# Kernel tuning notes

Measured on AMD Instinct MI355X. Metric: run time of the kernel, lower is better.

The kernel has to match this reference:

```python
import jax, jax.numpy as jnp
import numpy as np

ALPHA = 0.2      # leaky_alpha
GRAPH_ITR = 2    # graph_itr
ENC_LEN = 250    # output_begin_idx = encoder_sequence.shape[1]


def _char_embedding(ids, emb, conv_w, conv_b):
    # ids: [B,N,Wl] int -> char-CNN: embed, conv1d over word dim, relu, max-pool
    x = emb[ids]                                      # [B,N,Wl,E]
    B, N, Wl, E = x.shape
    x = x.reshape(B * N, Wl, E).transpose(0, 2, 1)    # [B*N, E, Wl]
    y = jax.lax.conv_general_dilated(x, conv_w, (1,), [(2, 2)],
                                     dimension_numbers=('NCH', 'OIH', 'NCH'))
    y = jax.nn.relu(y + conv_b[None, :, None])        # [B*N, F, Wl]
    return y.max(axis=2).reshape(B, N, -1)            # [B,N,F]


def _dynamic_graph(x, W0a, W0b, b0, W1, b1, Wout, bout):
    # Pairwise MLP on concat(x_i, x_j); first layer computed as split matmuls
    # so the [B,N,N,2d] concat is never materialized.
    hi = jnp.einsum('bnd,de->bne', x, W0a)            # [B,N,d]
    hj = jnp.einsum('bnd,de->bne', x, W0b)            # [B,N,d]
    h = jax.nn.relu(hi[:, :, None, :] + hj[:, None, :, :] + b0)   # [B,N,N,d]
    h = jax.nn.relu(jnp.einsum('bnme,ef->bnmf', h, W1) + b1)      # [B,N,N,d]
    return jax.nn.sigmoid(jnp.einsum('bnme,e->bnm', h, Wout[:, 0]) + bout[0])


def _gat(x, adj, W, a1, a2):
    # Multi-head GAT: per-head projection, additive attention, adjacency-masked softmax.
    Wh = jnp.einsum('bnd,hdk->bhnk', x, W)            # [B,H,N,hid]
    f1 = jnp.einsum('bhnk,hk->bhn', Wh, a1)
    f2 = jnp.einsum('bhnk,hk->bhn', Wh, a2)
    e = jax.nn.leaky_relu(f1[:, :, :, None] + f2[:, :, None, :], ALPHA)  # [B,H,N,N]
    e = jnp.where(adj[:, None, :, :] > 0, e, -9e15)
    attn = jax.nn.softmax(e, axis=-1)
    h = jax.nn.elu(jnp.einsum('bhnm,bhmk->bhnk', attn, Wh))
    B, H, N, K = h.shape
    return h.transpose(0, 2, 1, 3).reshape(B, N, H * K)  # concat heads -> [B,N,d]


def setup_inputs() -> dict:
    key = jax.random.key(0)
    ks = jax.random.split(key, 20)
    B, Le, Ld, Wl = 2, 250, 150, 16
    Vin, E, F, K = 128, 64, 128, 5
    H, hid, Vout = 8, 32, 5000
    d = H * hid  # 256
    s = lambda k, sh: jax.random.normal(k, sh, dtype=jnp.float32) * 0.05
    return {
        'encoder_sequence': jax.random.randint(ks[0], (B, Le, Wl), 0, Vin),
        'initial_decoder_sequence': jax.random.randint(ks[1], (B, Ld, Wl), 0, Vin),
        'fixed_graph': jax.random.randint(ks[2], (B, Le + Ld, Le + Ld), 0, 2),
        'char_emb': s(ks[3], (Vin, E)),
        'conv_w': s(ks[4], (F, E, K)),
        'conv_b': jnp.zeros((F,), jnp.float32),
        'hst_W': s(ks[5], (F, d)),
        'hst_b': jnp.zeros((d,), jnp.float32),
        'dg_W0a': s(ks[6], (d, d)),
        'dg_W0b': s(ks[7], (d, d)),
        'dg_b0': jnp.zeros((d,), jnp.float32),
        'dg_W1': s(ks[8], (d, d)),
        'dg_b1': jnp.zeros((d,), jnp.float32),
        'dg_Wout': s(ks[9], (d, 1)),
        'dg_bout': jnp.zeros((1,), jnp.float32),
        'att_W': s(ks[10], (H, d, hid)),
        'att_a1': s(ks[11], (H, hid)),
        'att_a2': s(ks[12], (H, hid)),
        'out_W': s(ks[13], (d, Vout)),
        'out_b': jnp.zeros((Vout,), jnp.float32),
    }


def reference(encoder_sequence, initial_decoder_sequence, fixed_graph,
              char_emb, conv_w, conv_b, hst_W, hst_b,
              dg_W0a, dg_W0b, dg_b0, dg_W1, dg_b1, dg_Wout, dg_bout,
              att_W, att_a1, att_a2, out_W, out_b):
    ids = jnp.concatenate([encoder_sequence, initial_decoder_sequence], axis=1)  # [B,N,Wl]
    x = _char_embedding(ids, char_emb, conv_w, conv_b)    # [B,N,F]
    x = x @ hst_W + hst_b                                 # [B,N,d]
    fixed = fixed_graph.astype(jnp.float32)
    for _ in range(GRAPH_ITR):
        dyn = _dynamic_graph(x, dg_W0a, dg_W0b, dg_b0, dg_W1, dg_b1, dg_Wout, dg_bout)
        adj = jnp.clip(dyn + fixed, 0.0, 1.0)             # combine dynamic + fixed graph
        x = _gat(x, adj, att_W, att_a1, att_a2)
    return x[:, ENC_LEN:, :] @ out_W + out_b              # [B, dec_len, Vout]
```

## Files before the change

kernel.cpp:

```cpp
#include <hip/hip_runtime.h>
#include <hip/hip_bf16.h>
#include <math.h>


__device__ __forceinline__ float bf2f_raw(unsigned int u) {
    union { unsigned int i; float f; } cv; cv.i = u << 16; return cv.f;
}

__global__ void k_table(const float* emb, const float* convw, float* T) {
    int v = blockIdx.x, f = threadIdx.x;
    __shared__ float er[64];
    if (f < 64) er[f] = emb[v * 64 + f];
    __syncthreads();
    float acc[5] = {0.f, 0.f, 0.f, 0.f, 0.f};
    const float* w = convw + f * 320;
    for (int e = 0; e < 64; ++e) {
        float xe = er[e];
#pragma unroll
        for (int k = 0; k < 5; ++k) acc[k] += xe * w[e * 5 + k];
    }
#pragma unroll
    for (int k = 0; k < 5; ++k) T[(k * 128 + v) * 128 + f] = acc[k];
}

__global__ void k_conv(const int* enc, const int* dec, const float* convb,
                       const float* T, float* xc) {
    int w = blockIdx.x;
    int b = w / 400, n = w % 400;
    __shared__ int ids[16];
    int f = threadIdx.x;
    if (f < 16) {
        ids[f] = (n < 250) ? enc[(b * 250 + n) * 16 + f]
                           : dec[(b * 150 + (n - 250)) * 16 + f];
    }
    __syncthreads();
    float best = -1e30f;
    for (int p = 0; p < 16; ++p) {
        float s = 0.f;
#pragma unroll
        for (int k = 0; k < 5; ++k) {
            int q = p + k - 2;
            if (q >= 0 && q < 16) s += T[(k * 128 + ids[q]) * 128 + f];
        }
        best = fmaxf(best, s);
    }
    xc[w * 128 + f] = fmaxf(best + convb[f], 0.f);
}

__global__ void k_hst(const float* xc, const float* W, const float* bias, float* x) {
    int w = blockIdx.x, t = threadIdx.x;
    __shared__ float xr[128];
    if (t < 128) xr[t] = xc[w * 128 + t];
    __syncthreads();
    float acc = bias[t];
    for (int c = 0; c < 128; ++c) acc += xr[c] * W[c * 256 + t];
    x[w * 256 + t] = acc;
}

__global__ __launch_bounds__(256) void k_wh(const float* x, const float* attW,
                                            const float* a1g, const float* a2g,
                                            float* Wh, float* f1, float* f2) {
    int blk = blockIdx.x, t = threadIdx.x;
    int w0 = blk * 2;
    int h = t >> 5, k = t & 31;
    __shared__ float xr[2][256];
    for (int i = t; i < 512; i += 256) xr[i >> 8][i & 255] = x[w0 * 256 + i];
    __syncthreads();
    float acc0 = 0.f, acc1 = 0.f;
    const float* Wp = attW + h * 8192 + k;
#pragma unroll 8
    for (int d = 0; d < 256; ++d) {
        float wv = Wp[d * 32];
        acc0 += xr[0][d] * wv;
        acc1 += xr[1][d] * wv;
    }
    float a1v = a1g[t], a2v = a2g[t];
    int b = w0 / 400;
    int bh = b * 8 + h;
    float accs[2] = {acc0, acc1};
#pragma unroll
    for (int rw = 0; rw < 2; ++rw) {
        int n = (w0 + rw) % 400;
        Wh[(bh * 400 + n) * 32 + k] = accs[rw];
        float v1 = accs[rw] * a1v, v2 = accs[rw] * a2v;
#pragma unroll
        for (int mm = 16; mm >= 1; mm >>= 1) {
            v1 += __shfl_xor(v1, mm, 64);
            v2 += __shfl_xor(v2, mm, 64);
        }
        if (k == 0) { f1[bh * 400 + n] = v1; f2[bh * 400 + n] = v2; }
    }
}

#define WST 36
__global__ __launch_bounds__(256) void k_attn(const float* Wh, const float* f1g,
                                              const float* f2g, float* xout) {
    int tile = blockIdx.x, bh = blockIdx.y;
    int b = bh >> 3, h = bh & 7;
    int t = threadIdx.x;
    int n0 = tile * 16;
    __shared__ float Whl[400 * WST];
    __shared__ float f2l[400];
    __shared__ float pl[4][400];
    __shared__ float f1l[16];
    __shared__ float red[4][8][4][4];
    __shared__ float sred[2][4][4];
    __shared__ float wmax[4];

    const float4* Whg4 = (const float4*)(Wh + bh * 12800);
    for (int i = t; i < 3200; i += 256) {
        float4 v = Whg4[i];
        int m = i >> 3, k4 = i & 7;
        *(float4*)&Whl[m * WST + k4 * 4] = v;
    }
    float fm = -1e30f;
    for (int m = t; m < 400; m += 256) {
        float v = f2g[bh * 400 + m];
        f2l[m] = v;
        fm = fmaxf(fm, v);
    }
    if (t < 16) f1l[t] = f1g[bh * 400 + n0 + t];
#pragma unroll
    for (int mm = 32; mm >= 1; mm >>= 1) fm = fmaxf(fm, __shfl_xor(fm, mm, 64));
    if ((t & 63) == 0) wmax[t >> 6] = fm;
    __syncthreads();
    float fmax2 = fmaxf(fmaxf(wmax[0], wmax[1]), fmaxf(wmax[2], wmax[3]));

    int g = t & 7, kq = (t >> 3) & 7, wv = t >> 6;
    int gm = g + 8 * wv;
    for (int it = 0; it < 4; ++it) {
        float ps[4];
#pragma unroll
        for (int rr = 0; rr < 4; ++rr) {
            float f1n = f1l[it * 4 + rr];
            float rowm = f1n + fmax2;
            rowm = rowm > 0.f ? rowm : 0.2f * rowm;
            float p_s = 0.f;
            for (int m = t; m < 400; m += 256) {
                float e = f1n + f2l[m];
                e = e > 0.f ? e : 0.2f * e;
                float p = __expf(e - rowm);
                pl[rr][m] = p;
                p_s += p;
            }
            ps[rr] = p_s;
        }
#pragma unroll
        for (int rr = 0; rr < 4; ++rr) {
            float v = ps[rr];
#pragma unroll
            for (int mm = 32; mm >= 1; mm >>= 1) v += __shfl_xor(v, mm, 64);
            if ((t & 63) == 0) sred[it & 1][rr][t >> 6] = v;
        }
        __syncthreads();
        float a[4][4];
#pragma unroll
        for (int rr = 0; rr < 4; ++rr)
#pragma unroll
            for (int c = 0; c < 4; ++c) a[rr][c] = 0.f;
        for (int m = gm; m < 400; m += 32) {
            float4 w4 = *(const float4*)&Whl[m * WST + kq * 4];
            float p0 = pl[0][m], p1 = pl[1][m], p2 = pl[2][m], p3 = pl[3][m];
            a[0][0] += p0 * w4.x; a[0][1] += p0 * w4.y; a[0][2] += p0 * w4.z; a[0][3] += p0 * w4.w;
            a[1][0] += p1 * w4.x; a[1][1] += p1 * w4.y; a[1][2] += p1 * w4.z; a[1][3] += p1 * w4.w;
            a[2][0] += p2 * w4.x; a[2][1] += p2 * w4.y; a[2][2] += p2 * w4.z; a[2][3] += p2 * w4.w;
            a[3][0] += p3 * w4.x; a[3][1] += p3 * w4.y; a[3][2] += p3 * w4.z; a[3][3] += p3 * w4.w;
        }
#pragma unroll
        for (int rr = 0; rr < 4; ++rr)
#pragma unroll
            for (int c = 0; c < 4; ++c) {
                float v = a[rr][c];
                v += __shfl_xor(v, 1, 64);
                v += __shfl_xor(v, 2, 64);
                v += __shfl_xor(v, 4, 64);
                a[rr][c] = v;
            }
        if (g == 0) {
#pragma unroll
            for (int rr = 0; rr < 4; ++rr)
#pragma unroll
                for (int c = 0; c < 4; ++c) red[wv][kq][rr][c] = a[rr][c];
        }
        __syncthreads();
        if (t < 128) {
            int rw3 = t >> 5, kk = t & 31;
            int q3 = kk >> 2, c3 = kk & 3;
            float s = sred[it & 1][rw3][0] + sred[it & 1][rw3][1]
                    + sred[it & 1][rw3][2] + sred[it & 1][rw3][3];
            float o = (red[0][q3][rw3][c3] + red[1][q3][rw3][c3]
                     + red[2][q3][rw3][c3] + red[3][q3][rw3][c3]) / s;
            o = o > 0.f ? o : (__expf(o) - 1.f);
            int n = n0 + it * 4 + rw3;
            xout[(b * 400 + n) * 256 + h * 32 + kk] = o;
        }
    }
}

__global__ void k_w2b(const float* W, unsigned short* Wb, int n) {
    int i = blockIdx.x * 256 + threadIdx.x;
    if (i < n) {
        __hip_bfloat16 h = __float2bfloat16(W[i]);
        Wb[i] = *reinterpret_cast<unsigned short*>(&h);
    }
}

__global__ __launch_bounds__(256) void k_out(const float* x, const unsigned short* Wb,
                                             const float* bias, float* out) {
    int vt = blockIdx.x, rg = blockIdx.y, t = threadIdx.x;
    __shared__ float xr[6][256];
    int r0 = rg * 6;
    int b = r0 / 150, n0 = 250 + (r0 % 150);
    for (int i = t; i < 1536; i += 256) {
        int rr = i >> 8, dd = i & 255;
        xr[rr][dd] = x[(b * 400 + n0 + rr) * 256 + dd];
    }
    __syncthreads();
    int v = vt * 512 + t * 2;
    if (v >= 5000) return;
    float acc[6][2];
#pragma unroll
    for (int rr = 0; rr < 6; ++rr) { acc[rr][0] = 0.f; acc[rr][1] = 0.f; }
    const unsigned short* Wp = Wb + v;
#pragma unroll 8
    for (int dd = 0; dd < 256; ++dd) {
        unsigned int wu = *reinterpret_cast<const unsigned int*>(Wp + dd * 5000);
        float w0 = bf2f_raw(wu & 0xFFFFu);
        float w1 = bf2f_raw(wu >> 16);
#pragma unroll
        for (int rr = 0; rr < 6; ++rr) {
            float xv = xr[rr][dd];
            acc[rr][0] += xv * w0;
            acc[rr][1] += xv * w1;
        }
    }
    float b0 = bias[v], b1 = bias[v + 1];
#pragma unroll
    for (int rr = 0; rr < 6; ++rr) {
        out[(r0 + rr) * 5000 + v]     = acc[rr][0] + b0;
        out[(r0 + rr) * 5000 + v + 1] = acc[rr][1] + b1;
    }
}

extern "C" void kernel_launch(void* const* d_in, const int* in_sizes, int n_in,
                              void* d_out, int out_size, void* d_ws, size_t ws_size,
                              hipStream_t stream) {
    const int*   enc   = (const int*)d_in[0];
    const int*   dec   = (const int*)d_in[1];
    const float* emb   = (const float*)d_in[3];
    const float* convw = (const float*)d_in[4];
    const float* convb = (const float*)d_in[5];
    const float* hstW  = (const float*)d_in[6];
    const float* hstb  = (const float*)d_in[7];
    const float* attW  = (const float*)d_in[15];
    const float* a1    = (const float*)d_in[16];
    const float* a2    = (const float*)d_in[17];
    const float* outW  = (const float*)d_in[18];
    const float* outb  = (const float*)d_in[19];
    float* out = (float*)d_out;

    char* ws = (char*)d_ws;
    float* T   = (float*)ws; ws += 5 * 128 * 128 * 4;
    float* xc  = (float*)ws; ws += 800 * 128 * 4;
    float* xA  = (float*)ws; ws += 800 * 256 * 4;
    float* xB  = (float*)ws; ws += 800 * 256 * 4;
    float* Wh  = (float*)ws; ws += 16 * 400 * 32 * 4;
    float* f1  = (float*)ws; ws += 16 * 400 * 4;
    float* f2  = (float*)ws; ws += 16 * 400 * 4;
    unsigned short* Wb = (unsigned short*)ws; ws += 256 * 5000 * 2;

    k_w2b<<<5000, 256, 0, stream>>>(outW, Wb, 256 * 5000);
    k_table<<<128, 128, 0, stream>>>(emb, convw, T);
    k_conv<<<800, 128, 0, stream>>>(enc, dec, convb, T, xc);
    k_hst<<<800, 256, 0, stream>>>(xc, hstW, hstb, xA);

    float* xin = xA;
    float* xo  = xB;
    for (int it = 0; it < 2; ++it) {
        k_wh<<<400, 256, 0, stream>>>(xin, attW, a1, a2, Wh, f1, f2);
        k_attn<<<dim3(25, 16), 256, 0, stream>>>(Wh, f1, f2, xo);
        float* tmp = xin; xin = xo; xo = tmp;
    }
    k_out<<<dim3(10, 50), 256, 0, stream>>>(xin, Wb, outb, out);
}
```

Before: 115.2 us.

## Fuse prep and conv+projection kernels, pack attention probabilities as float4

Combines the char-conv lookup table build and the bf16 weight conversion into one launch, with the conversion now packing two values per thread. The conv and linear projection are fused so the intermediate stays in shared memory and is never written to global memory. In the attention kernel, the four rows' probabilities are computed in one pass over f2 and stored interleaved as float4, so the accumulation loop does one shared load per m instead of four. The aim is fewer kernel launches and less global and shared-memory traffic, at the cost of a larger block size for the fused conv kernel.

After: 103.5 us. 1.11x faster.

```diff
diff --git a/kernel.cpp b/kernel.cpp
--- a/kernel.cpp
+++ b/kernel.cpp
@@ -6,54 +6,70 @@
 __device__ __forceinline__ float bf2f_raw(unsigned int u) {
     union { unsigned int i; float f; } cv; cv.i = u << 16; return cv.f;
 }
-
-__global__ void k_table(const float* emb, const float* convw, float* T) {
-    int v = blockIdx.x, f = threadIdx.x;
-    __shared__ float er[64];
-    if (f < 64) er[f] = emb[v * 64 + f];
-    __syncthreads();
-    float acc[5] = {0.f, 0.f, 0.f, 0.f, 0.f};
-    const float* w = convw + f * 320;
-    for (int e = 0; e < 64; ++e) {
-        float xe = er[e];
-#pragma unroll
-        for (int k = 0; k < 5; ++k) acc[k] += xe * w[e * 5 + k];
-    }
-#pragma unroll
-    for (int k = 0; k < 5; ++k) T[(k * 128 + v) * 128 + f] = acc[k];
-}
-
-__global__ void k_conv(const int* enc, const int* dec, const float* convb,
-                       const float* T, float* xc) {
-    int w = blockIdx.x;
+__device__ __forceinline__ unsigned short f2bf(float f) {
+    __hip_bfloat16 h = __float2bfloat16(f);
+    return *reinterpret_cast<unsigned short*>(&h);
+}
+
+__global__ __launch_bounds__(256) void k_prep(const float* emb, const float* convw,
+                                              float* T, const float* W,
+                                              unsigned short* Wb) {
+    int bid = blockIdx.x, t = threadIdx.x;
+    if (bid < 128) {
+        int v = bid;
+        __shared__ float er[64];
+        if (t < 64) er[t] = emb[v * 64 + t];
+        __syncthreads();
+        if (t < 128) {
+            float acc[5] = {0.f, 0.f, 0.f, 0.f, 0.f};
+            const float* w = convw + t * 320;
+            for (int e = 0; e < 64; ++e) {
+                float xe = er[e];
+#pragma unroll
+                for (int k = 0; k < 5; ++k) acc[k] += xe * w[e * 5 + k];
+            }
+#pragma unroll
+            for (int k = 0; k < 5; ++k) T[(k * 128 + v) * 128 + t] = acc[k];
+        }
+    } else {
+        int i0 = (bid - 128) * 512 + t * 2;
+        if (i0 < 256 * 5000) {
+            float2 w2 = *reinterpret_cast<const float2*>(W + i0);
+            unsigned int u = ((unsigned int)f2bf(w2.y) << 16) | f2bf(w2.x);
+            *reinterpret_cast<unsigned int*>(Wb + i0) = u;
+        }
+    }
+}
+
+__global__ __launch_bounds__(256) void k_convhst(const int* enc, const int* dec,
+                                                 const float* convb, const float* T,
+                                                 const float* hstW, const float* hstb,
+                                                 float* x) {
+    int w = blockIdx.x, t = threadIdx.x;
     int b = w / 400, n = w % 400;
     __shared__ int ids[16];
-    int f = threadIdx.x;
-    if (f < 16) {
-        ids[f] = (n < 250) ? enc[(b * 250 + n) * 16 + f]
-                           : dec[(b * 150 + (n - 250)) * 16 + f];
-    }
-    __syncthreads();
-    float best = -1e30f;
-    for (int p = 0; p < 16; ++p) {
-        float s = 0.f;
-#pragma unroll
-        for (int k = 0; k < 5; ++k) {
-            int q = p + k - 2;
-            if (q >= 0 && q < 16) s += T[(k * 128 + ids[q]) * 128 + f];
-        }
-        best = fmaxf(best, s);
-    }
-    xc[w * 128 + f] = fmaxf(best + convb[f], 0.f);
-}
-
-__global__ void k_hst(const float* xc, const float* W, const float* bias, float* x) {
-    int w = blockIdx.x, t = threadIdx.x;
-    __shared__ float xr[128];
-    if (t < 128) xr[t] = xc[w * 128 + t];
-    __syncthreads();
-    float acc = bias[t];
-    for (int c = 0; c < 128; ++c) acc += xr[c] * W[c * 256 + t];
+    __shared__ float xcl[128];
+    if (t < 16) {
+        ids[t] = (n < 250) ? enc[(b * 250 + n) * 16 + t]
+                           : dec[(b * 150 + (n - 250)) * 16 + t];
+    }
+    __syncthreads();
+    if (t < 128) {
+        float best = -1e30f;
+        for (int p = 0; p < 16; ++p) {
+            float s = 0.f;
+#pragma unroll
+            for (int k = 0; k < 5; ++k) {
+                int q = p + k - 2;
+                if (q >= 0 && q < 16) s += T[(k * 128 + ids[q]) * 128 + t];
+            }
+            best = fmaxf(best, s);
+        }
+        xcl[t] = fmaxf(best + convb[t], 0.f);
+    }
+    __syncthreads();
+    float acc = hstb[t];
+    for (int c = 0; c < 128; ++c) acc += xcl[c] * hstW[c * 256 + t];
     x[w * 256 + t] = acc;
 }
 
@@ -101,7 +117,7 @@
     int n0 = tile * 16;
     __shared__ float Whl[400 * WST];
     __shared__ float f2l[400];
-    __shared__ float pl[4][400];
+    __shared__ float4 plT[400];
     __shared__ float f1l[16];
     __shared__ float red[4][8][4][4];
     __shared__ float sred[2][4][4];
@@ -129,28 +145,40 @@
     int g = t & 7, kq = (t >> 3) & 7, wv = t >> 6;
     int gm = g + 8 * wv;
     for (int it = 0; it < 4; ++it) {
-        float ps[4];
-#pragma unroll
-        for (int rr = 0; rr < 4; ++rr) {
-            float f1n = f1l[it * 4 + rr];
-            float rowm = f1n + fmax2;
-            rowm = rowm > 0.f ? rowm : 0.2f * rowm;
-            float p_s = 0.f;
-            for (int m = t; m < 400; m += 256) {
-                float e = f1n + f2l[m];
-                e = e > 0.f ? e : 0.2f * e;
-                float p = __expf(e - rowm);
-                pl[rr][m] = p;
-                p_s += p;
-            }
-            ps[rr] = p_s;
-        }
-#pragma unroll
-        for (int rr = 0; rr < 4; ++rr) {
-            float v = ps[rr];
-#pragma unroll
-            for (int mm = 32; mm >= 1; mm >>= 1) v += __shfl_xor(v, mm, 64);
-            if ((t & 63) == 0) sred[it & 1][rr][t >> 6] = v;
+        float f1a = f1l[it * 4 + 0], f1b = f1l[it * 4 + 1];
+        float f1c = f1l[it * 4 + 2], f1d = f1l[it * 4 + 3];
+        float rm0 = f1a + fmax2; rm0 = rm0 > 0.f ? rm0 : 0.2f * rm0;
+        float rm1 = f1b + fmax2; rm1 = rm1 > 0.f ? rm1 : 0.2f * rm1;
+        float rm2 = f1c + fmax2; rm2 = rm2 > 0.f ? rm2 : 0.2f * rm2;
+        float rm3 = f1d + fmax2; rm3 = rm3 > 0.f ? rm3 : 0.2f * rm3;
+        float ps0 = 0.f, ps1 = 0.f, ps2 = 0.f, ps3 = 0.f;
+        for (int m = t; m < 400; m += 256) {
+            float f2v = f2l[m];
+            float e0 = f1a + f2v; e0 = e0 > 0.f ? e0 : 0.2f * e0;
+            float e1 = f1b + f2v; e1 = e1 > 0.f ? e1 : 0.2f * e1;
+            float e2 = f1c + f2v; e2 = e2 > 0.f ? e2 : 0.2f * e2;
+            float e3 = f1d + f2v; e3 = e3 > 0.f ? e3 : 0.2f * e3;
+            float4 pv;
+            pv.x = __expf(e0 - rm0); ps0 += pv.x;
+            pv.y = __expf(e1 - rm1); ps1 += pv.y;
+            pv.z = __expf(e2 - rm2); ps2 += pv.z;
+            pv.w = __expf(e3 - rm3); ps3 += pv.w;
+            plT[m] = pv;
+        }
+        {
+            float v0 = ps0, v1 = ps1, v2 = ps2, v3 = ps3;
+#pragma unroll
+            for (int mm = 32; mm >= 1; mm >>= 1) {
+                v0 += __shfl_xor(v0, mm, 64);
+                v1 += __shfl_xor(v1, mm, 64);
+                v2 += __shfl_xor(v2, mm, 64);
+                v3 += __shfl_xor(v3, mm, 64);
+            }
+            if ((t & 63) == 0) {
+                int wq = t >> 6;
+                sred[it & 1][0][wq] = v0; sred[it & 1][1][wq] = v1;
+                sred[it & 1][2][wq] = v2; sred[it & 1][3][wq] = v3;
+            }
         }
         __syncthreads();
         float a[4][4];
@@ -160,11 +188,11 @@
             for (int c = 0; c < 4; ++c) a[rr][c] = 0.f;
         for (int m = gm; m < 400; m += 32) {
             float4 w4 = *(const float4*)&Whl[m * WST + kq * 4];
-            float p0 = pl[0][m], p1 = pl[1][m], p2 = pl[2][m], p3 = pl[3][m];
-            a[0][0] += p0 * w4.x; a[0][1] += p0 * w4.y; a[0][2] += p0 * w4.z; a[0][3] += p0 * w4.w;
-            a[1][0] += p1 * w4.x; a[1][1] += p1 * w4.y; a[1][2] += p1 * w4.z; a[1][3] += p1 * w4.w;
-            a[2][0] += p2 * w4.x; a[2][1] += p2 * w4.y; a[2][2] += p2 * w4.z; a[2][3] += p2 * w4.w;
-            a[3][0] += p3 * w4.x; a[3][1] += p3 * w4.y; a[3][2] += p3 * w4.z; a[3][3] += p3 * w4.w;
+            float4 p4 = plT[m];
+            a[0][0] += p4.x * w4.x; a[0][1] += p4.x * w4.y; a[0][2] += p4.x * w4.z; a[0][3] += p4.x * w4.w;
+            a[1][0] += p4.y * w4.x; a[1][1] += p4.y * w4.y; a[1][2] += p4.y * w4.z; a[1][3] += p4.y * w4.w;
+            a[2][0] += p4.z * w4.x; a[2][1] += p4.z * w4.y; a[2][2] += p4.z * w4.z; a[2][3] += p4.z * w4.w;
+            a[3][0] += p4.w * w4.x; a[3][1] += p4.w * w4.y; a[3][2] += p4.w * w4.z; a[3][3] += p4.w * w4.w;
         }
 #pragma unroll
         for (int rr = 0; rr < 4; ++rr)
@@ -194,14 +222,6 @@
             int n = n0 + it * 4 + rw3;
             xout[(b * 400 + n) * 256 + h * 32 + kk] = o;
         }
-    }
-}
-
-__global__ void k_w2b(const float* W, unsigned short* Wb, int n) {
-    int i = blockIdx.x * 256 + threadIdx.x;
-    if (i < n) {
-        __hip_bfloat16 h = __float2bfloat16(W[i]);
-        Wb[i] = *reinterpret_cast<unsigned short*>(&h);
     }
 }
 
@@ -261,7 +281,6 @@
 
     char* ws = (char*)d_ws;
     float* T   = (float*)ws; ws += 5 * 128 * 128 * 4;
-    float* xc  = (float*)ws; ws += 800 * 128 * 4;
     float* xA  = (float*)ws; ws += 800 * 256 * 4;
     float* xB  = (float*)ws; ws += 800 * 256 * 4;
     float* Wh  = (float*)ws; ws += 16 * 400 * 32 * 4;
@@ -269,10 +288,8 @@
     float* f2  = (float*)ws; ws += 16 * 400 * 4;
     unsigned short* Wb = (unsigned short*)ws; ws += 256 * 5000 * 2;
 
-    k_w2b<<<5000, 256, 0, stream>>>(outW, Wb, 256 * 5000);
-    k_table<<<128, 128, 0, stream>>>(emb, convw, T);
-    k_conv<<<800, 128, 0, stream>>>(enc, dec, convb, T, xc);
-    k_hst<<<800, 256, 0, stream>>>(xc, hstW, hstb, xA);
+    k_prep<<<2628, 256, 0, stream>>>(emb, convw, T, outW, Wb);
+    k_convhst<<<800, 256, 0, stream>>>(enc, dec, convb, T, hstW, hstb, xA);
 
     float* xin = xA;
     float* xo  = xB;
```
